# Kernel tuning notes

Measured on AMD Instinct MI355X. Metric: run time of the kernel, lower is better.

## Reference

```python
import jax, jax.numpy as jnp
import numpy as np

INPUT_DIM = 512
SMOOTH_FACTOR = 1.0
NOISE_THRESHOLD = 0.0
TAIL_THRESHOLD = 0.45


def setup_inputs() -> dict:
    key = jax.random.key(0)
    k1, k2, k3, k4, k5 = jax.random.split(key, 5)
    B, T, D = 16, 4096, INPUT_DIM
    hidden = jax.random.normal(k1, (B, T, D), dtype=jnp.float32)
    mask = jnp.ones((B, 1, T), dtype=jnp.float32)
    # Conv1d(D, D, kernel=3) weight [out, in, k], Linear(D, 1) weight [1, D]
    conv_w = jax.random.normal(k2, (D, D, 3), dtype=jnp.float32) * (1.0 / np.sqrt(D * 3))
    conv_b = jax.random.normal(k3, (D,), dtype=jnp.float32) * 0.01
    out_w = jax.random.normal(k4, (1, D), dtype=jnp.float32) * (1.0 / np.sqrt(D))
    out_b = jax.random.normal(k5, (1,), dtype=jnp.float32) * 0.01
    return dict(hidden=hidden, mask=mask, conv_w=conv_w, conv_b=conv_b,
                out_w=out_w, out_b=out_b)


def _cif(hidden, alphas):
    """Vectorized continuous integrate-and-fire.
    hidden: [B, T1, D], alphas: [B, T1] -> padded frames [B, T1, D].
    Equivalent to the torch boolean-mask gather/roll/scatter version: for the
    k-th fire at time t_k, frame_k = Q[t_k] - Q[t_{k-1}] where
    Q[t] = cumsum(alpha*h)[t] - frac(cumsum(alpha))[t] * h[t].
    """
    B, T1, D = hidden.shape
    ps = jnp.cumsum(alphas, axis=1)                      # prefix sum of alphas
    psf = jnp.floor(ps)
    prev_psf = jnp.concatenate([jnp.zeros((B, 1), psf.dtype), psf[:, :-1]], axis=1)
    fire = (psf - prev_psf) > 0                          # [B, T1] bool, fire indicator
    frac = ps - psf                                      # remains at each position
    P = jnp.cumsum(alphas[..., None] * hidden, axis=1)   # [B, T1, D]
    Q = P - frac[..., None] * hidden                     # boundary-adjusted prefix
    k = jnp.cumsum(fire.astype(jnp.int32), axis=1) - 1   # fire ordinal per position
    idx = jnp.where(fire, k, T1)                         # dump non-fires to extra slot
    upd = jnp.where(fire[..., None], Q, 0.0)
    Qs = jnp.zeros((B, T1 + 1, D), hidden.dtype).at[jnp.arange(B)[:, None], idx].add(upd)[:, :T1]
    frames = Qs - jnp.concatenate([jnp.zeros((B, 1, D), hidden.dtype), Qs[:, :-1]], axis=1)
    batch_len = fire.sum(axis=1)                         # number of fires per batch
    valid = jnp.arange(T1)[None, :] < batch_len[:, None]
    return jnp.where(valid[..., None], frames, 0.0)


def reference(hidden, mask, conv_w, conv_b, out_w, out_b):
    B, T, D = hidden.shape
    # conv over time with pad (l_order=1, r_order=1), kernel 3, then ReLU
    x = jnp.transpose(hidden, (0, 2, 1))                 # [B, D, T]
    y = jax.lax.conv_general_dilated(x, conv_w, (1,), [(1, 1)],
                                     dimension_numbers=('NCH', 'OIH', 'NCH'))
    y = jax.nn.relu(y + conv_b[None, :, None])
    y = jnp.transpose(y, (0, 2, 1))                      # [B, T, D]
    o = y @ out_w.T + out_b                              # [B, T, 1]
    alphas = jax.nn.relu(jax.nn.sigmoid(o) * SMOOTH_FACTOR - NOISE_THRESHOLD)
    mk = jnp.transpose(mask, (0, 2, 1))                  # [B, T, 1]
    alphas = (alphas * mk)[..., 0]                       # [B, T]
    mk2 = mk[..., 0]                                     # [B, T]
    # tail_process_fn: add tail_threshold at first padded position
    zeros_t = jnp.zeros((B, 1), alphas.dtype)
    ones_t = jnp.ones((B, 1), alphas.dtype)
    mask_1 = jnp.concatenate([mk2, zeros_t], axis=1)     # [B, T+1]
    mask_2 = jnp.concatenate([ones_t, mk2], axis=1)
    tail = (mask_2 - mask_1) * TAIL_THRESHOLD
    alphas = jnp.concatenate([alphas, zeros_t], axis=1) + tail   # [B, T+1]
    h = jnp.concatenate([hidden, jnp.zeros((B, 1, D), hidden.dtype)], axis=1)
    token_num = jnp.floor(alphas.sum(-1))                # [B]
    acoustic = _cif(h, alphas)                           # [B, T+1, D] zero-padded
    # data-dependent truncation (eager, matches torch .item())
    token_num_int = int(np.asarray(jnp.max(token_num)).astype(np.int32))
    acoustic = acoustic[:, :token_num_int, :]
    return acoustic, token_num, alphas
```

## Files before the change

### kernel.cpp

```cpp
#include <hip/hip_runtime.h>
#include <math.h>

#define B_ 16
#define T_ 4096
#define D_ 512
#define T1_ 4097
#define NTHR 512

#define SMOOTH_FACTOR 1.0
#define NOISE_THRESHOLD 0.0
#define TAIL_THRESHOLD 0.45

typedef short bf16x8 __attribute__((ext_vector_type(8)));
typedef float f32x16 __attribute__((ext_vector_type(16)));
union U4 { uint4 u; bf16x8 s; };

#define WB_OFF   ((size_t)0)
#define PART_OFF ((size_t)3145728)
#define A64_OFF  ((size_t)7340032)
#define FT_OFF   ((size_t)7864448)
#define FF_OFF   ((size_t)8126656)
#define LEN_OFF  ((size_t)8651072)

__device__ __forceinline__ unsigned bf_rne(unsigned x) {
    return (x + 0x7FFFu + ((x >> 16) & 1u)) >> 16;
}

__global__ void k_wt(const float* __restrict__ cw, uint4* __restrict__ wb) {
    int idx = blockIdx.x * 256 + threadIdx.x;
    if (idx >= 196608) return;
    int o  = idx & 511;
    int r  = idx >> 9;
    int kg = r & 1;
    int rc = r >> 1;
    int comp = rc / 96;
    int c    = rc - comp * 96;
    unsigned uw[4];
    #pragma unroll
    for (int j = 0; j < 4; ++j) {
        unsigned short us[2];
        #pragma unroll
        for (int q = 0; q < 2; ++q) {
            int e = j * 2 + q;
            int k = c * 16 + kg * 8 + e;
            int tap = k >> 9, i = k & 511;
            float v = cw[((size_t)o * D_ + i) * 3 + tap];
            unsigned x  = __float_as_uint(v);
            unsigned hi = bf_rne(x);
            if (comp == 0) us[q] = (unsigned short)hi;
            else {
                float rem = v - __uint_as_float(hi << 16);
                us[q] = (unsigned short)bf_rne(__float_as_uint(rem));
            }
        }
        uw[j] = (unsigned)us[0] | ((unsigned)us[1] << 16);
    }
    wb[idx] = make_uint4(uw[0], uw[1], uw[2], uw[3]);
}

__global__ __launch_bounds__(NTHR)
void k_conv(const float* __restrict__ h, const uint4* __restrict__ wb,
            const float* __restrict__ cbp, const float* __restrict__ owp,
            double* __restrict__ part) {
    extern __shared__ uint4 lds[];
    uint4* Ahi = lds;
    uint4* Ami = lds + 130 * 33;

    const int tid  = threadIdx.x;
    const int b    = blockIdx.y;
    const int t0   = blockIdx.x * 128;
    const int lane = tid & 63;
    const int w    = tid >> 6;
    const int l31  = lane & 31;
    const int kg   = lane >> 5;

    const float* hb = h + (size_t)b * T_ * D_;

    f32x16 c0a = {0,0,0,0,0,0,0,0,0,0,0,0,0,0,0,0};
    f32x16 c0b = c0a, c1a = c0a, c1b = c0a, c2a = c0a, c2b = c0a, c3a = c0a, c3b = c0a;

    const uint4* wp0h = wb + ((size_t)kg * 512 + w * 64 + l31);
    const uint4* wp1h = wp0h + 32;
    const uint4* wp0m = wp0h + 98304;
    const uint4* wp1m = wp1h + 98304;

    U4 w0hA, w1hA, w0mA, w1mA, w0hB, w1hB, w0mB, w1mB;
    U4 ah0A, am0A, ah1A, am1A, ah0B, am0B, ah1B, am1B;
    U4 ah2, am2, ah3, am3;

    #define LOADW(PH, Q, W0H, W1H, W0M, W1M) {                                   \
        size_t c_ = (size_t)((((Q) >> 4) << 5) + (PH) * 16 + ((Q) & 15)) * 1024; \
        W0H.u = wp0h[c_];  W1H.u = wp1h[c_];                                     \
        W0M.u = wp0m[c_];  W1M.u = wp1m[c_]; }

    #define LOADA01(Q, AH0, AM0, AH1, AM1) {                       \
        int ia_ = (l31 + ((Q) >> 4)) * 33 + (((Q) & 15) << 1) + kg; \
        AH0.u = Ahi[ia_];            AM0.u = Ami[ia_];             \
        AH1.u = Ahi[ia_ + 32 * 33];  AM1.u = Ami[ia_ + 32 * 33]; }

    #define LOADA23(Q) {                                            \
        int ia_ = (l31 + ((Q) >> 4)) * 33 + (((Q) & 15) << 1) + kg; \
        ah2.u = Ahi[ia_ + 64 * 33];  am2.u = Ami[ia_ + 64 * 33];   \
        ah3.u = Ahi[ia_ + 96 * 33];  am3.u = Ami[ia_ + 96 * 33]; }

    #define MF3(AH, AM, CA, CB, W0H, W1H, W0M, W1M) {                             \
        CA = __builtin_amdgcn_mfma_f32_32x32x16_bf16(AH.s, W0H.s, CA, 0, 0, 0);   \
        CB = __builtin_amdgcn_mfma_f32_32x32x16_bf16(AH.s, W1H.s, CB, 0, 0, 0);   \
        CA = __builtin_amdgcn_mfma_f32_32x32x16_bf16(AH.s, W0M.s, CA, 0, 0, 0);   \
        CB = __builtin_amdgcn_mfma_f32_32x32x16_bf16(AH.s, W1M.s, CB, 0, 0, 0);   \
        CA = __builtin_amdgcn_mfma_f32_32x32x16_bf16(AM.s, W0H.s, CA, 0, 0, 0);   \
        CB = __builtin_amdgcn_mfma_f32_32x32x16_bf16(AM.s, W1H.s, CB, 0, 0, 0); }

    LOADW(0, 0, w0hA, w1hA, w0mA, w1mA);

    for (int ph = 0; ph < 2; ++ph) {
        if (ph) __syncthreads();
        {
            float4 x0, x1, y0, y1;
            int idx = tid;
            {
                int r = idx >> 5, cu4 = idx & 31, t = t0 - 1 + r;
                if (t >= 0 && t < T_) {
                    const float* p = hb + (size_t)t * D_ + ph * 256 + cu4 * 8;
                    x0 = *(const float4*)p; x1 = *(const float4*)(p + 4);
                } else { x0 = x1 = make_float4(0.f, 0.f, 0.f, 0.f); }
            }
            for (int it = 0; it < 9; ++it) {
                int nidx = idx + 512;
                if (it < 8 && nidx < 4160) {
                    int r = nidx >> 5, cu4 = nidx & 31, t = t0 - 1 + r;
                    if (t >= 0 && t < T_) {
                        const float* p = hb + (size_t)t * D_ + ph * 256 + cu4 * 8;
                        y0 = *(const float4*)p; y1 = *(const float4*)(p + 4);
                    } else { y0 = y1 = make_float4(0.f, 0.f, 0.f, 0.f); }
                }
                if (idx < 4160) {
                    float v[8] = {x0.x, x0.y, x0.z, x0.w, x1.x, x1.y, x1.z, x1.w};
                    unsigned hw[4], mw[4];
                    #pragma unroll
                    for (int j = 0; j < 4; ++j) {
                        unsigned short hs_[2], ms_[2];
                        #pragma unroll
                        for (int q = 0; q < 2; ++q) {
                            float f = v[j * 2 + q];
                            unsigned hi = bf_rne(__float_as_uint(f));
                            float rem = f - __uint_as_float(hi << 16);
                            hs_[q] = (unsigned short)hi;
                            ms_[q] = (unsigned short)bf_rne(__float_as_uint(rem));
                        }
                        hw[j] = hs_[0] | ((unsigned)hs_[1] << 16);
                        mw[j] = ms_[0] | ((unsigned)ms_[1] << 16);
                    }
                    int r = idx >> 5, cu4 = idx & 31;
                    Ahi[r * 33 + cu4] = make_uint4(hw[0], hw[1], hw[2], hw[3]);
                    Ami[r * 33 + cu4] = make_uint4(mw[0], mw[1], mw[2], mw[3]);
                }
                x0 = y0; x1 = y1; idx = nidx;
            }
        }
        __syncthreads();

        LOADA01(0, ah0A, am0A, ah1A, am1A);

        for (int q = 0; q < 48; q += 2) {
            LOADA23(q);
            LOADW(ph, q + 1, w0hB, w1hB, w0mB, w1mB);
            LOADA01(q + 1, ah0B, am0B, ah1B, am1B);
            MF3(ah0A, am0A, c0a, c0b, w0hA, w1hA, w0mA, w1mA);
            MF3(ah1A, am1A, c1a, c1b, w0hA, w1hA, w0mA, w1mA);
            MF3(ah2,  am2,  c2a, c2b, w0hA, w1hA, w0mA, w1mA);
            MF3(ah3,  am3,  c3a, c3b, w0hA, w1hA, w0mA, w1mA);
            LOADA23(q + 1);
            if (q + 2 < 48) {
                LOADW(ph, q + 2, w0hA, w1hA, w0mA, w1mA);
                LOADA01(q + 2, ah0A, am0A, ah1A, am1A);
            } else if (ph == 0) {
                LOADW(1, 0, w0hA, w1hA, w0mA, w1mA);
            }
            MF3(ah0B, am0B, c0a, c0b, w0hB, w1hB, w0mB, w1mB);
            MF3(ah1B, am1B, c1a, c1b, w0hB, w1hB, w0mB, w1mB);
            MF3(ah2,  am2,  c2a, c2b, w0hB, w1hB, w0mB, w1mB);
            MF3(ah3,  am3,  c3a, c3b, w0hB, w1hB, w0mB, w1mB);
        }
    }
    #undef LOADW
    #undef LOADA01
    #undef LOADA23
    #undef MF3

    const int o0 = w * 64 + l31, o1 = o0 + 32;
    const double cb0 = (double)cbp[o0], cb1 = (double)cbp[o1];
    const double ow0 = (double)owp[o0], ow1 = (double)owp[o1];
    #pragma unroll
    for (int s = 0; s < 4; ++s) {
        const f32x16 aca = (s == 0) ? c0a : (s == 1) ? c1a : (s == 2) ? c2a : c3a;
        const f32x16 acb = (s == 0) ? c0b : (s == 1) ? c1b : (s == 2) ? c2b : c3b;
        #pragma unroll
        for (int v = 0; v < 16; ++v) {
            double z0 = (double)aca[v] + cb0; z0 = z0 > 0.0 ? z0 : 0.0;
            double z1 = (double)acb[v] + cb1; z1 = z1 > 0.0 ? z1 : 0.0;
            double p = fma(ow0, z0, ow1 * z1);
            #pragma unroll
            for (int off = 1; off < 32; off <<= 1) p += __shfl_xor(p, off);
            if (l31 == 0) {
                int m = (v & 3) + 8 * (v >> 2) + 4 * kg;
                part[((size_t)b * T_ + t0 + s * 32 + m) * 8 + w] = p;
            }
        }
    }
}

__global__ void k_alpha(const double* __restrict__ part, const float* __restrict__ mask,
                        const float* __restrict__ outb,
                        float* __restrict__ out_alpha, double* __restrict__ a64) {
    int gid = blockIdx.x * 256 + threadIdx.x;
    if (gid >= B_ * T1_) return;
    int b = gid / T1_;
    int t = gid - b * T1_;
    double a;
    if (t < T_) {
        double o = (double)outb[0];
        #pragma unroll
        for (int j = 0; j < 8; ++j)
            o += part[((size_t)b * T_ + t) * 8 + j];
        double s = 1.0 / (1.0 + exp(-o));
        double ap = s * SMOOTH_FACTOR - NOISE_THRESHOLD;
        if (ap < 0.0) ap = 0.0;
        double mk = (double)mask[b * T_ + t];
        double mprev = (t == 0) ? 1.0 : (double)mask[b * T_ + t - 1];
        a = ap * mk + TAIL_THRESHOLD * (mprev - mk);
    } else {
        a = TAIL_THRESHOLD * (double)mask[b * T_ + T_ - 1];
    }
    out_alpha[gid] = (float)a;
    a64[gid] = a;
}

__global__ void k_scan(const double* __restrict__ a64,
                       float* __restrict__ out_tok, int* __restrict__ fire_t,
                       double* __restrict__ fire_frac, int* __restrict__ blen) {
    const int b = blockIdx.x;
    const int lane = threadIdx.x;
    const double* ab = a64 + (size_t)b * T1_;
    double carry = 0.0;
    int nf = 0;

    double a = ab[lane];
    for (int c = 0; c < 65; ++c) {
        int t = c * 64 + lane;
        int tn = t + 64;
        double anext = (tn <= T_ && c < 64) ? ab[tn] : 0.0;
        double x = a;
        #pragma unroll
        for (int off = 1; off < 64; off <<= 1) {
            double y = __shfl_up(x, off);
            if (lane >= off) x += y;
        }
        double ps = carry + x;
        double ps_prev = __shfl_up(ps, 1);
        if (lane == 0) ps_prev = carry;
        double psf = floor(ps), ppsf = floor(ps_prev);
        bool fire = (t <= T_) && (psf > ppsf);
        unsigned long long m = __ballot(fire);
        if (fire) {
            int k = nf + (int)__popcll(m & ((1ull << lane) - 1ull));
            fire_t[(size_t)b * T1_ + k] = t;
            fire_frac[(size_t)b * T1_ + k] = ps - psf;
        }
        nf += (int)__popcll(m);
        carry = __shfl(ps, 63);
        a = anext;
    }
    if (lane == 0) {
        blen[b] = nf;
        out_tok[b] = (float)floor(carry);
    }
}

__global__ void k_frames(const float* __restrict__ h, const double* __restrict__ a64,
                         const int* __restrict__ fire_t, const double* __restrict__ fire_frac,
                         const int* __restrict__ blen, float* __restrict__ out, int K) {
    const int k = blockIdx.x;
    const int b = blockIdx.y;
    const int tid = threadIdx.x;
    double ax = 0.0, ay = 0.0, az = 0.0, aw = 0.0;
    const int len = blen[b];
    if (k < len) {
        const int t1 = fire_t[(size_t)b * T1_ + k];
        const int t0 = (k > 0) ? fire_t[(size_t)b * T1_ + k - 1] : -1;
        const double f1 = fire_frac[(size_t)b * T1_ + k];
        const double f0 = (k > 0) ? fire_frac[(size_t)b * T1_ + k - 1] : 0.0;
        if (t0 >= 0 && t0 < T_) {
            float4 hv = *(const float4*)(h + ((size_t)b * T_ + t0) * D_ + (tid << 2));
            ax = fma(f0, (double)hv.x, ax); ay = fma(f0, (double)hv.y, ay);
            az = fma(f0, (double)hv.z, az); aw = fma(f0, (double)hv.w, aw);
        }
        for (int t = t0 + 1; t <= t1; ++t) {
            if (t >= T_) break;
            double c = a64[(size_t)b * T1_ + t] - ((t == t1) ? f1 : 0.0);
            float4 hv = *(const float4*)(h + ((size_t)b * T_ + t) * D_ + (tid << 2));
            ax = fma(c, (double)hv.x, ax); ay = fma(c, (double)hv.y, ay);
            az = fma(c, (double)hv.z, az); aw = fma(c, (double)hv.w, aw);
        }
    }
    float4 o = make_float4((float)ax, (float)ay, (float)az, (float)aw);
    *(float4*)(out + ((size_t)b * K + k) * D_ + (tid << 2)) = o;
}

extern "C" void kernel_launch(void* const* d_in, const int* in_sizes, int n_in,
                              void* d_out, int out_size, void* d_ws, size_t ws_size,
                              hipStream_t stream) {
    const float* h    = (const float*)d_in[0];
    const float* mask = (const float*)d_in[1];
    const float* cw   = (const float*)d_in[2];
    const float* cb   = (const float*)d_in[3];
    const float* ow   = (const float*)d_in[4];
    const float* ob   = (const float*)d_in[5];

    char* ws = (char*)d_ws;
    uint4*  wb        = (uint4*)(ws + WB_OFF);
    double* part      = (double*)(ws + PART_OFF);
    double* a64       = (double*)(ws + A64_OFF);
    int*    fire_t    = (int*)(ws + FT_OFF);
    double* fire_frac = (double*)(ws + FF_OFF);
    int*    blen      = (int*)(ws + LEN_OFF);

    long long K = ((long long)out_size - B_ - (long long)B_ * T1_) / ((long long)B_ * D_);
    if (K < 1) K = 1;
    float* out_ac    = (float*)d_out;
    float* out_tok   = out_ac + (size_t)B_ * K * D_;
    float* out_alpha = out_tok + B_;

    const int lds = 2 * 130 * 33 * 16;
    (void)hipFuncSetAttribute((const void*)k_conv,
                              hipFuncAttributeMaxDynamicSharedMemorySize, lds);

    k_wt<<<dim3(768), dim3(256), 0, stream>>>(cw, wb);
    k_conv<<<dim3(T_ / 128, B_), dim3(NTHR), lds, stream>>>(h, wb, cb, ow, part);
    k_alpha<<<dim3((B_ * T1_ + 255) / 256), dim3(256), 0, stream>>>(part, mask, ob,
                                                                    out_alpha, a64);
    k_scan<<<dim3(B_), dim3(64), 0, stream>>>(a64, out_tok, fire_t, fire_frac, blen);
    k_frames<<<dim3((unsigned)K, B_), dim3(128), 0, stream>>>(h, a64, fire_t, fire_frac,
                                                              blen, out_ac, (int)K);
}
```

Baseline: 345.0 us.

## Retile conv to 64-row blocks with 1024 threads and fuse alpha epilogue

The conv kernel now processes 64 time rows per block with 1024 threads (16 waves, each owning 32 output channels) and loads the full 512-wide input tile into LDS once instead of in two phases. The per-wave partial dot products with the output weight are reduced through LDS inside the block, so the sigmoid/mask alpha computation happens in the conv epilogue and the separate alpha kernel and its global partials buffer are removed. The tail alpha element moves into the scan kernel. In exchange, each weight fragment loaded from memory is reused across fewer rows, so weight traffic per block is higher relative to compute. The larger blocks may also limit how many waves can be resident.

Measured after the change: 416.6 us. 20.8% more time.

```diff
diff --git a/kernel.cpp b/kernel.cpp
--- a/kernel.cpp
+++ b/kernel.cpp
@@ -5,7 +5,7 @@
 #define T_ 4096
 #define D_ 512
 #define T1_ 4097
-#define NTHR 512
+#define NTHR 1024
 
 #define SMOOTH_FACTOR 1.0
 #define NOISE_THRESHOLD 0.0
@@ -16,11 +16,10 @@
 union U4 { uint4 u; bf16x8 s; };
 
 #define WB_OFF   ((size_t)0)
-#define PART_OFF ((size_t)3145728)
-#define A64_OFF  ((size_t)7340032)
-#define FT_OFF   ((size_t)7864448)
-#define FF_OFF   ((size_t)8126656)
-#define LEN_OFF  ((size_t)8651072)
+#define A64_OFF  ((size_t)3145728)
+#define FT_OFF   ((size_t)3670144)
+#define FF_OFF   ((size_t)3932352)
+#define LEN_OFF  ((size_t)4456768)
 
 __device__ __forceinline__ unsigned bf_rne(unsigned x) {
     return (x + 0x7FFFu + ((x >> 16) & 1u)) >> 16;
@@ -61,14 +60,15 @@
 __global__ __launch_bounds__(NTHR)
 void k_conv(const float* __restrict__ h, const uint4* __restrict__ wb,
             const float* __restrict__ cbp, const float* __restrict__ owp,
-            double* __restrict__ part) {
+            const float* __restrict__ mask, const float* __restrict__ obp,
+            float* __restrict__ out_alpha, double* __restrict__ a64) {
     extern __shared__ uint4 lds[];
     uint4* Ahi = lds;
-    uint4* Ami = lds + 130 * 33;
+    uint4* Ami = lds + 66 * 65;
 
     const int tid  = threadIdx.x;
     const int b    = blockIdx.y;
-    const int t0   = blockIdx.x * 128;
+    const int t0   = blockIdx.x * 64;
     const int lane = tid & 63;
     const int w    = tid >> 6;
     const int l31  = lane & 31;
@@ -76,169 +76,138 @@
 
     const float* hb = h + (size_t)b * T_ * D_;
 
-    f32x16 c0a = {0,0,0,0,0,0,0,0,0,0,0,0,0,0,0,0};
-    f32x16 c0b = c0a, c1a = c0a, c1b = c0a, c2a = c0a, c2b = c0a, c3a = c0a, c3b = c0a;
-
-    const uint4* wp0h = wb + ((size_t)kg * 512 + w * 64 + l31);
-    const uint4* wp1h = wp0h + 32;
-    const uint4* wp0m = wp0h + 98304;
-    const uint4* wp1m = wp1h + 98304;
-
-    U4 w0hA, w1hA, w0mA, w1mA, w0hB, w1hB, w0mB, w1mB;
+    {
+        float4 x0, x1, y0, y1;
+        int idx = tid;
+        if (idx < 4224) {
+            int r = idx >> 6, cu4 = idx & 63, t = t0 - 1 + r;
+            if (t >= 0 && t < T_) {
+                const float* p = hb + (size_t)t * D_ + cu4 * 8;
+                x0 = *(const float4*)p; x1 = *(const float4*)(p + 4);
+            } else { x0 = x1 = make_float4(0.f, 0.f, 0.f, 0.f); }
+        }
+        for (int it = 0; it < 5; ++it) {
+            int nidx = idx + 1024;
+            if (it < 4 && nidx < 4224) {
+                int r = nidx >> 6, cu4 = nidx & 63, t = t0 - 1 + r;
+                if (t >= 0 && t < T_) {
+                    const float* p = hb + (size_t)t * D_ + cu4 * 8;
+                    y0 = *(const float4*)p; y1 = *(const float4*)(p + 4);
+                } else { y0 = y1 = make_float4(0.f, 0.f, 0.f, 0.f); }
+            }
+            if (idx < 4224) {
+                float v[8] = {x0.x, x0.y, x0.z, x0.w, x1.x, x1.y, x1.z, x1.w};
+                unsigned hw[4], mw[4];
+                #pragma unroll
+                for (int j = 0; j < 4; ++j) {
+                    unsigned short hs_[2], ms_[2];
+                    #pragma unroll
+                    for (int q = 0; q < 2; ++q) {
+                        float f = v[j * 2 + q];
+                        unsigned hi = bf_rne(__float_as_uint(f));
+                        float rem = f - __uint_as_float(hi << 16);
+                        hs_[q] = (unsigned short)hi;
+                        ms_[q] = (unsigned short)bf_rne(__float_as_uint(rem));
+                    }
+                    hw[j] = hs_[0] | ((unsigned)hs_[1] << 16);
+                    mw[j] = ms_[0] | ((unsigned)ms_[1] << 16);
+                }
+                int r = idx >> 6, cu4 = idx & 63;
+                Ahi[r * 65 + cu4] = make_uint4(hw[0], hw[1], hw[2], hw[3]);
+                Ami[r * 65 + cu4] = make_uint4(mw[0], mw[1], mw[2], mw[3]);
+            }
+            x0 = y0; x1 = y1; idx = nidx;
+        }
+    }
+    __syncthreads();
+
+    f32x16 acc0 = {0,0,0,0,0,0,0,0,0,0,0,0,0,0,0,0};
+    f32x16 acc1 = acc0;
+
+    const uint4* wph = wb + ((size_t)kg * 512 + w * 32 + l31);
+    const uint4* wpm = wph + 98304;
+
+    U4 whA, wmA, whB, wmB;
     U4 ah0A, am0A, ah1A, am1A, ah0B, am0B, ah1B, am1B;
-    U4 ah2, am2, ah3, am3;
-
-    #define LOADW(PH, Q, W0H, W1H, W0M, W1M) {                                   \
-        size_t c_ = (size_t)((((Q) >> 4) << 5) + (PH) * 16 + ((Q) & 15)) * 1024; \
-        W0H.u = wp0h[c_];  W1H.u = wp1h[c_];                                     \
-        W0M.u = wp0m[c_];  W1M.u = wp1m[c_]; }
-
-    #define LOADA01(Q, AH0, AM0, AH1, AM1) {                       \
-        int ia_ = (l31 + ((Q) >> 4)) * 33 + (((Q) & 15) << 1) + kg; \
-        AH0.u = Ahi[ia_];            AM0.u = Ami[ia_];             \
-        AH1.u = Ahi[ia_ + 32 * 33];  AM1.u = Ami[ia_ + 32 * 33]; }
-
-    #define LOADA23(Q) {                                            \
-        int ia_ = (l31 + ((Q) >> 4)) * 33 + (((Q) & 15) << 1) + kg; \
-        ah2.u = Ahi[ia_ + 64 * 33];  am2.u = Ami[ia_ + 64 * 33];   \
-        ah3.u = Ahi[ia_ + 96 * 33];  am3.u = Ami[ia_ + 96 * 33]; }
-
-    #define MF3(AH, AM, CA, CB, W0H, W1H, W0M, W1M) {                             \
-        CA = __builtin_amdgcn_mfma_f32_32x32x16_bf16(AH.s, W0H.s, CA, 0, 0, 0);   \
-        CB = __builtin_amdgcn_mfma_f32_32x32x16_bf16(AH.s, W1H.s, CB, 0, 0, 0);   \
-        CA = __builtin_amdgcn_mfma_f32_32x32x16_bf16(AH.s, W0M.s, CA, 0, 0, 0);   \
-        CB = __builtin_amdgcn_mfma_f32_32x32x16_bf16(AH.s, W1M.s, CB, 0, 0, 0);   \
-        CA = __builtin_amdgcn_mfma_f32_32x32x16_bf16(AM.s, W0H.s, CA, 0, 0, 0);   \
-        CB = __builtin_amdgcn_mfma_f32_32x32x16_bf16(AM.s, W1H.s, CB, 0, 0, 0); }
-
-    LOADW(0, 0, w0hA, w1hA, w0mA, w1mA);
-
-    for (int ph = 0; ph < 2; ++ph) {
-        if (ph) __syncthreads();
-        {
-            float4 x0, x1, y0, y1;
-            int idx = tid;
-            {
-                int r = idx >> 5, cu4 = idx & 31, t = t0 - 1 + r;
-                if (t >= 0 && t < T_) {
-                    const float* p = hb + (size_t)t * D_ + ph * 256 + cu4 * 8;
-                    x0 = *(const float4*)p; x1 = *(const float4*)(p + 4);
-                } else { x0 = x1 = make_float4(0.f, 0.f, 0.f, 0.f); }
-            }
-            for (int it = 0; it < 9; ++it) {
-                int nidx = idx + 512;
-                if (it < 8 && nidx < 4160) {
-                    int r = nidx >> 5, cu4 = nidx & 31, t = t0 - 1 + r;
-                    if (t >= 0 && t < T_) {
-                        const float* p = hb + (size_t)t * D_ + ph * 256 + cu4 * 8;
-                        y0 = *(const float4*)p; y1 = *(const float4*)(p + 4);
-                    } else { y0 = y1 = make_float4(0.f, 0.f, 0.f, 0.f); }
-                }
-                if (idx < 4160) {
-                    float v[8] = {x0.x, x0.y, x0.z, x0.w, x1.x, x1.y, x1.z, x1.w};
-                    unsigned hw[4], mw[4];
-                    #pragma unroll
-                    for (int j = 0; j < 4; ++j) {
-                        unsigned short hs_[2], ms_[2];
-                        #pragma unroll
-                        for (int q = 0; q < 2; ++q) {
-                            float f = v[j * 2 + q];
-                            unsigned hi = bf_rne(__float_as_uint(f));
-                            float rem = f - __uint_as_float(hi << 16);
-                            hs_[q] = (unsigned short)hi;
-                            ms_[q] = (unsigned short)bf_rne(__float_as_uint(rem));
-                        }
-                        hw[j] = hs_[0] | ((unsigned)hs_[1] << 16);
-                        mw[j] = ms_[0] | ((unsigned)ms_[1] << 16);
-                    }
-                    int r = idx >> 5, cu4 = idx & 31;
-                    Ahi[r * 33 + cu4] = make_uint4(hw[0], hw[1], hw[2], hw[3]);
-                    Ami[r * 33 + cu4] = make_uint4(mw[0], mw[1], mw[2], mw[3]);
-                }
-                x0 = y0; x1 = y1; idx = nidx;
-            }
-        }
-        __syncthreads();
-
-        LOADA01(0, ah0A, am0A, ah1A, am1A);
-
-        for (int q = 0; q < 48; q += 2) {
-            LOADA23(q);
-            LOADW(ph, q + 1, w0hB, w1hB, w0mB, w1mB);
-            LOADA01(q + 1, ah0B, am0B, ah1B, am1B);
-            MF3(ah0A, am0A, c0a, c0b, w0hA, w1hA, w0mA, w1mA);
-            MF3(ah1A, am1A, c1a, c1b, w0hA, w1hA, w0mA, w1mA);
-            MF3(ah2,  am2,  c2a, c2b, w0hA, w1hA, w0mA, w1mA);
-            MF3(ah3,  am3,  c3a, c3b, w0hA, w1hA, w0mA, w1mA);
-            LOADA23(q + 1);
-            if (q + 2 < 48) {
-                LOADW(ph, q + 2, w0hA, w1hA, w0mA, w1mA);
-                LOADA01(q + 2, ah0A, am0A, ah1A, am1A);
-            } else if (ph == 0) {
-                LOADW(1, 0, w0hA, w1hA, w0mA, w1mA);
-            }
-            MF3(ah0B, am0B, c0a, c0b, w0hB, w1hB, w0mB, w1mB);
-            MF3(ah1B, am1B, c1a, c1b, w0hB, w1hB, w0mB, w1mB);
-            MF3(ah2,  am2,  c2a, c2b, w0hB, w1hB, w0mB, w1mB);
-            MF3(ah3,  am3,  c3a, c3b, w0hB, w1hB, w0mB, w1mB);
-        }
+
+    #define LOADW(Q, WH, WM) {                 \
+        size_t c_ = (size_t)(Q) * 1024;        \
+        WH.u = wph[c_];  WM.u = wpm[c_]; }
+
+    #define LOADA(Q, AH0, AM0, AH1, AM1) {                              \
+        int ia_ = (l31 + ((Q) >> 5)) * 65 + (((Q) & 31) << 1) + kg;     \
+        AH0.u = Ahi[ia_];            AM0.u = Ami[ia_];                  \
+        AH1.u = Ahi[ia_ + 32 * 65];  AM1.u = Ami[ia_ + 32 * 65]; }
+
+    #define MF3(AH, AM, CC, WH, WM) {                                           \
+        CC = __builtin_amdgcn_mfma_f32_32x32x16_bf16(AH.s, WH.s, CC, 0, 0, 0);  \
+        CC = __builtin_amdgcn_mfma_f32_32x32x16_bf16(AH.s, WM.s, CC, 0, 0, 0);  \
+        CC = __builtin_amdgcn_mfma_f32_32x32x16_bf16(AM.s, WH.s, CC, 0, 0, 0); }
+
+    LOADW(0, whA, wmA);
+    LOADW(1, whB, wmB);
+    LOADA(0, ah0A, am0A, ah1A, am1A);
+
+    for (int q = 0; q < 96; q += 2) {
+        LOADA(q + 1, ah0B, am0B, ah1B, am1B);
+        MF3(ah0A, am0A, acc0, whA, wmA);
+        MF3(ah1A, am1A, acc1, whA, wmA);
+        if (q + 2 < 96) {
+            LOADW(q + 2, whA, wmA);
+            LOADA(q + 2, ah0A, am0A, ah1A, am1A);
+        }
+        MF3(ah0B, am0B, acc0, whB, wmB);
+        MF3(ah1B, am1B, acc1, whB, wmB);
+        if (q + 3 < 96) LOADW(q + 3, whB, wmB);
     }
     #undef LOADW
-    #undef LOADA01
-    #undef LOADA23
+    #undef LOADA
     #undef MF3
 
-    const int o0 = w * 64 + l31, o1 = o0 + 32;
-    const double cb0 = (double)cbp[o0], cb1 = (double)cbp[o1];
-    const double ow0 = (double)owp[o0], ow1 = (double)owp[o1];
+    const int o = w * 32 + l31;
+    const double cbv = (double)cbp[o];
+    const double owv = (double)owp[o];
+    __syncthreads();
+    double* pw = (double*)lds;
+
     #pragma unroll
-    for (int s = 0; s < 4; ++s) {
-        const f32x16 aca = (s == 0) ? c0a : (s == 1) ? c1a : (s == 2) ? c2a : c3a;
-        const f32x16 acb = (s == 0) ? c0b : (s == 1) ? c1b : (s == 2) ? c2b : c3b;
+    for (int s = 0; s < 2; ++s) {
+        const f32x16 ac = s ? acc1 : acc0;
         #pragma unroll
         for (int v = 0; v < 16; ++v) {
-            double z0 = (double)aca[v] + cb0; z0 = z0 > 0.0 ? z0 : 0.0;
-            double z1 = (double)acb[v] + cb1; z1 = z1 > 0.0 ? z1 : 0.0;
-            double p = fma(ow0, z0, ow1 * z1);
+            double z = (double)ac[v] + cbv;
+            z = z > 0.0 ? z : 0.0;
+            double p = owv * z;
             #pragma unroll
             for (int off = 1; off < 32; off <<= 1) p += __shfl_xor(p, off);
             if (l31 == 0) {
                 int m = (v & 3) + 8 * (v >> 2) + 4 * kg;
-                part[((size_t)b * T_ + t0 + s * 32 + m) * 8 + w] = p;
+                pw[w * 64 + s * 32 + m] = p;
             }
         }
     }
-}
-
-__global__ void k_alpha(const double* __restrict__ part, const float* __restrict__ mask,
-                        const float* __restrict__ outb,
-                        float* __restrict__ out_alpha, double* __restrict__ a64) {
-    int gid = blockIdx.x * 256 + threadIdx.x;
-    if (gid >= B_ * T1_) return;
-    int b = gid / T1_;
-    int t = gid - b * T1_;
-    double a;
-    if (t < T_) {
-        double o = (double)outb[0];
+    __syncthreads();
+
+    if (tid < 64) {
+        int t = t0 + tid;
+        double osum = (double)obp[0];
         #pragma unroll
-        for (int j = 0; j < 8; ++j)
-            o += part[((size_t)b * T_ + t) * 8 + j];
-        double s = 1.0 / (1.0 + exp(-o));
-        double ap = s * SMOOTH_FACTOR - NOISE_THRESHOLD;
+        for (int j = 0; j < 16; ++j) osum += pw[j * 64 + tid];
+        double sg = 1.0 / (1.0 + exp(-osum));
+        double ap = sg * SMOOTH_FACTOR - NOISE_THRESHOLD;
         if (ap < 0.0) ap = 0.0;
         double mk = (double)mask[b * T_ + t];
         double mprev = (t == 0) ? 1.0 : (double)mask[b * T_ + t - 1];
-        a = ap * mk + TAIL_THRESHOLD * (mprev - mk);
-    } else {
-        a = TAIL_THRESHOLD * (double)mask[b * T_ + T_ - 1];
-    }
-    out_alpha[gid] = (float)a;
-    a64[gid] = a;
-}
-
-__global__ void k_scan(const double* __restrict__ a64,
-                       float* __restrict__ out_tok, int* __restrict__ fire_t,
-                       double* __restrict__ fire_frac, int* __restrict__ blen) {
+        double a = ap * mk + TAIL_THRESHOLD * (mprev - mk);
+        out_alpha[(size_t)b * T1_ + t] = (float)a;
+        a64[(size_t)b * T1_ + t] = a;
+    }
+}
+
+__global__ void k_scan(const double* __restrict__ a64, const float* __restrict__ mask,
+                       float* __restrict__ out_tok, float* __restrict__ out_alpha,
+                       int* __restrict__ fire_t, double* __restrict__ fire_frac,
+                       int* __restrict__ blen) {
     const int b = blockIdx.x;
     const int lane = threadIdx.x;
     const double* ab = a64 + (size_t)b * T1_;
@@ -248,8 +217,14 @@
     double a = ab[lane];
     for (int c = 0; c < 65; ++c) {
         int t = c * 64 + lane;
+        if (t == T_) {
+            a = TAIL_THRESHOLD * (double)mask[b * T_ + T_ - 1];
+            out_alpha[(size_t)b * T1_ + T_] = (float)a;
+        } else if (t > T_) {
+            a = 0.0;
+        }
         int tn = t + 64;
-        double anext = (tn <= T_ && c < 64) ? ab[tn] : 0.0;
+        double anext = (tn < T_) ? ab[tn] : 0.0;
         double x = a;
         #pragma unroll
         for (int off = 1; off < 64; off <<= 1) {
@@ -319,7 +294,6 @@
 
     char* ws = (char*)d_ws;
     uint4*  wb        = (uint4*)(ws + WB_OFF);
-    double* part      = (double*)(ws + PART_OFF);
     double* a64       = (double*)(ws + A64_OFF);
     int*    fire_t    = (int*)(ws + FT_OFF);
     double* fire_frac = (double*)(ws + FF_OFF);
@@ -331,15 +305,15 @@
     float* out_tok   = out_ac + (size_t)B_ * K * D_;
     float* out_alpha = out_tok + B_;
 
-    const int lds = 2 * 130 * 33 * 16;
+    const int lds = 2 * 66 * 65 * 16;
     (void)hipFuncSetAttribute((const void*)k_conv,
                               hipFuncAttributeMaxDynamicSharedMemorySize, lds);
 
     k_wt<<<dim3(768), dim3(256), 0, stream>>>(cw, wb);
-    k_conv<<<dim3(T_ / 128, B_), dim3(NTHR), lds, stream>>>(h, wb, cb, ow, part);
-    k_alpha<<<dim3((B_ * T1_ + 255) / 256), dim3(256), 0, stream>>>(part, mask, ob,
-                                                                    out_alpha, a64);
-    k_scan<<<dim3(B_), dim3(64), 0, stream>>>(a64, out_tok, fire_t, fire_frac, blen);
+    k_conv<<<dim3(T_ / 64, B_), dim3(NTHR), lds, stream>>>(h, wb, cb, ow, mask, ob,
+                                                           out_alpha, a64);
+    k_scan<<<dim3(B_), dim3(64), 0, stream>>>(a64, mask, out_tok, out_alpha,
+                                              fire_t, fire_frac, blen);
     k_frames<<<dim3((unsigned)K, B_), dim3(128), 0, stream>>>(h, a64, fire_t, fire_frac,
                                                               blen, out_ac, (int)K);
 }
```
